# Kernel optimization log

Hardware: AMD Instinct MI355X
Metric: run time of the kernel (lower is better)

Reference implementation:

```python
import jax, jax.numpy as jnp
import numpy as np

N_NODES = 100_000
N_EDGES = 600_000
D = 128  # in_channels


def setup_inputs() -> dict:
    key = jax.random.key(0)
    k1, k2, k3, k4, k5 = jax.random.split(key, 5)
    node_embs_src = jax.random.normal(k1, (N_NODES, D), dtype=jnp.float32)
    node_embs_dst = jax.random.normal(k2, (N_NODES, D), dtype=jnp.float32)
    edge_index = jax.random.randint(k3, (2, N_EDGES), 0, N_NODES, dtype=jnp.int64)
    # MLP params: Linear(2D -> D), Linear(D -> 1); scaled like default torch init
    W1 = jax.random.normal(k4, (2 * D, D), dtype=jnp.float32) / np.sqrt(2 * D)
    b1 = jnp.zeros((D,), dtype=jnp.float32)
    W2 = jax.random.normal(k5, (D, 1), dtype=jnp.float32) / np.sqrt(D)
    b2 = jnp.zeros((1,), dtype=jnp.float32)
    return {
        "node_embs_src": node_embs_src,
        "node_embs_dst": node_embs_dst,
        "edge_index": edge_index,
        "W1": W1,
        "b1": b1,
        "W2": W2,
        "b2": b2,
    }


def reference(node_embs_src, node_embs_dst, edge_index, W1, b1, W2, b2):
    # Gather per-edge source / destination embeddings: [E, D] each
    src = node_embs_src[edge_index[0]]
    dst = node_embs_dst[edge_index[1]]
    # concat([src, dst]) @ W1 == src @ W1[:D] + dst @ W1[D:]  (avoids materializing [E, 2D])
    h = jnp.dot(src, W1[:D]) + jnp.dot(dst, W1[D:]) + b1  # [E, D]
    h = jax.nn.relu(h)
    logits = jnp.dot(h, W2) + b2  # [E, 1]
    return jax.nn.sigmoid(logits)
```

## Files before the change

kernel.cpp:

```cpp
#include <hip/hip_runtime.h>
#include <stdint.h>

typedef __attribute__((ext_vector_type(8))) short short8;
typedef __attribute__((ext_vector_type(4))) float f32x4;

__device__ __forceinline__ unsigned short f2bf(float f) {
  union { float f; uint32_t u; } v; v.f = f;
  uint32_t u = v.u;
  uint32_t r = (u + 0x7FFFu + ((u >> 16) & 1u)) >> 16;
  return (unsigned short)r;
}
__device__ __forceinline__ float bf2f(unsigned short h) {
  union { uint32_t u; float f; } v; v.u = ((uint32_t)h) << 16; return v.f;
}

#define NBM 64
__global__ __launch_bounds__(256, 4)
void node_phase_kernel(const float* __restrict__ src_emb,
                       const float* __restrict__ dst_emb,
                       const float* __restrict__ W1,
                       unsigned short* __restrict__ UV,
                       int Nn, int ntiles) {
  __shared__ __align__(16) char Als[NBM * 256];

  const int tbl = blockIdx.y;
  const float* emb = tbl ? dst_emb : src_emb;
  const float* Wt  = W1 + (size_t)tbl * 128 * 128;
  unsigned short* outp = UV + (size_t)tbl * Nn * 128;

  const int tid  = threadIdx.x;
  const int lane = tid & 63;
  const int w    = tid >> 6;
  const int l15  = lane & 15;
  const int lk8  = (lane >> 4) * 8;

  short8 bfrag[4][2];
#pragma unroll
  for (int s = 0; s < 4; ++s) {
#pragma unroll
    for (int nf = 0; nf < 2; ++nf) {
      const int col = w * 32 + 2 * l15 + nf;
      short8 t;
#pragma unroll
      for (int j = 0; j < 8; ++j) {
        const int k = s * 32 + lk8 + j;
        t[j] = (short)f2bf(Wt[k * 128 + col]);
      }
      bfrag[s][nf] = t;
    }
  }

  const int q = tid & 15, r0 = tid >> 4;
  const int swz = (l15 & 7) << 4;
  const int gx = gridDim.x;

  float4 p0[4], p1[4];
#pragma unroll
  for (int i = 0; i < 4; ++i) {
    const int node = blockIdx.x * NBM + i * 16 + r0;
    if (node < Nn) {
      const float* base = emb + (size_t)node * 128 + q * 8;
      p0[i] = *(const float4*)base;
      p1[i] = *(const float4*)(base + 4);
    }
  }

  for (int t = blockIdx.x; t < ntiles; t += gx) {
    const int t0 = t * NBM;

#pragma unroll
    for (int i = 0; i < 4; ++i) {
      const int row = i * 16 + r0;
      short8 hv;
      hv[0] = (short)f2bf(p0[i].x); hv[1] = (short)f2bf(p0[i].y);
      hv[2] = (short)f2bf(p0[i].z); hv[3] = (short)f2bf(p0[i].w);
      hv[4] = (short)f2bf(p1[i].x); hv[5] = (short)f2bf(p1[i].y);
      hv[6] = (short)f2bf(p1[i].z); hv[7] = (short)f2bf(p1[i].w);
      const int byteoff = row * 256 + ((q * 16) ^ ((row & 7) << 4));
      *(short8*)(Als + byteoff) = hv;
    }
    __syncthreads();

    const int tn = t + gx;
    if (tn < ntiles) {
#pragma unroll
      for (int i = 0; i < 4; ++i) {
        const int node = tn * NBM + i * 16 + r0;
        if (node < Nn) {
          const float* base = emb + (size_t)node * 128 + q * 8;
          p0[i] = *(const float4*)base;
          p1[i] = *(const float4*)(base + 4);
        }
      }
    }

#pragma unroll
    for (int m = 0; m < 4; ++m) {
      f32x4 acc0 = {0.f, 0.f, 0.f, 0.f};
      f32x4 acc1 = {0.f, 0.f, 0.f, 0.f};
      const int rowb = (m * 16 + l15) * 256;
      const int kb0  = lk8 * 2;
#pragma unroll
      for (int s = 0; s < 4; ++s) {
        const int off = rowb + ((s * 64 + kb0) ^ swz);
        const short8 a = *(const short8*)(Als + off);
        acc0 = __builtin_amdgcn_mfma_f32_16x16x32_bf16(a, bfrag[s][0], acc0, 0, 0, 0);
        acc1 = __builtin_amdgcn_mfma_f32_16x16x32_bf16(a, bfrag[s][1], acc1, 0, 0, 0);
      }
      const int col0 = w * 32 + 2 * l15;
#pragma unroll
      for (int reg = 0; reg < 4; ++reg) {
        const int orow = t0 + m * 16 + ((lane >> 4) * 4) + reg;
        if (orow < Nn) {
          const uint32_t pk = (uint32_t)f2bf(acc0[reg]) |
                              ((uint32_t)f2bf(acc1[reg]) << 16);
          *(uint32_t*)&outp[(size_t)orow * 128 + col0] = pk;
        }
      }
    }
    __syncthreads();
  }
}

__global__ __launch_bounds__(256, 8)
void edge_phase_kernel(const unsigned short* __restrict__ UV,
                       const int* __restrict__ eidx,
                       const float* __restrict__ b1,
                       const float* __restrict__ W2,
                       const float* __restrict__ b2,
                       float* __restrict__ out,
                       int E, int Nn) {
  const int tid = threadIdx.x;
  const int l15 = tid & 15;
  const int sg  = tid >> 4;

  float b1s[8], w2s[8];
#pragma unroll
  for (int j = 0; j < 8; ++j) {
    b1s[j] = b1[l15 * 8 + j];
    w2s[j] = W2[l15 * 8 + j];
  }
  const float b2s = b2[0];
  const unsigned short* U = UV;
  const unsigned short* V = UV + (size_t)Nn * 128;
  const int stride = gridDim.x * 16;

#pragma unroll 2
  for (int e = blockIdx.x * 16 + sg; e < E; e += stride) {
    const int s = eidx[e];
    const int d = eidx[E + e];
    const short8 u8 = *(const short8*)(U + (size_t)s * 128 + l15 * 8);
    const short8 v8 = *(const short8*)(V + (size_t)d * 128 + l15 * 8);
    float acc = 0.f;
#pragma unroll
    for (int j = 0; j < 8; ++j) {
      float g = bf2f((unsigned short)u8[j]) + bf2f((unsigned short)v8[j]) + b1s[j];
      g = g > 0.f ? g : 0.f;
      acc = fmaf(g, w2s[j], acc);
    }
#pragma unroll
    for (int off = 1; off < 16; off <<= 1)
      acc += __shfl_xor(acc, off, 64);
    if (l15 == 0) out[e] = 1.f / (1.f + __expf(-acc));
  }
}

#define BM 64
__global__ __launch_bounds__(256, 4)
void edge_decoder_fused(const float* __restrict__ src_emb,
                        const float* __restrict__ dst_emb,
                        const int* __restrict__ eidx,
                        const float* __restrict__ W1,
                        const float* __restrict__ b1,
                        const float* __restrict__ W2,
                        const float* __restrict__ b2,
                        float* __restrict__ out,
                        int E, int ntiles) {
  __shared__ __align__(16) char Als[BM * 512];
  __shared__ float rowpart[4][BM];

  const int tid  = threadIdx.x;
  const int lane = tid & 63;
  const int w    = tid >> 6;
  const int l15  = lane & 15;
  const int lk8  = (lane >> 4) * 8;

  short8 bfrag[8][2];
#pragma unroll
  for (int s = 0; s < 8; ++s) {
#pragma unroll
    for (int nf = 0; nf < 2; ++nf) {
      const int col = w * 32 + nf * 16 + l15;
      short8 t;
#pragma unroll
      for (int j = 0; j < 8; ++j) {
        const int k = s * 32 + lk8 + j;
        t[j] = (short)f2bf(W1[k * 128 + col]);
      }
      bfrag[s][nf] = t;
    }
  }
  float b1v[2], w2v[2];
#pragma unroll
  for (int nf = 0; nf < 2; ++nf) {
    const int col = w * 32 + nf * 16 + l15;
    b1v[nf] = b1[col];
    w2v[nf] = W2[col];
  }
  const float b2s = b2[0];

  const int q  = tid & 31;
  const int r0 = tid >> 5;
  const int qq = q & 15;
  const bool is_src = (q < 16);
  const int swz = (l15 & 7) << 4;

  for (int t = blockIdx.x; t < ntiles; t += gridDim.x) {
    const int t0 = t * BM;
#pragma unroll
    for (int i = 0; i < 8; ++i) {
      const int row = i * 8 + r0;
      const int e = t0 + row;
      if (e < E) {
        const int node = is_src ? eidx[e] : eidx[E + e];
        const float* base = (is_src ? src_emb : dst_emb) + (size_t)node * 128 + qq * 8;
        const float4 f0 = *(const float4*)base;
        const float4 f1 = *(const float4*)(base + 4);
        short8 hv;
        hv[0] = (short)f2bf(f0.x); hv[1] = (short)f2bf(f0.y);
        hv[2] = (short)f2bf(f0.z); hv[3] = (short)f2bf(f0.w);
        hv[4] = (short)f2bf(f1.x); hv[5] = (short)f2bf(f1.y);
        hv[6] = (short)f2bf(f1.z); hv[7] = (short)f2bf(f1.w);
        const int byteoff = row * 512 + ((q * 16) ^ ((row & 7) << 4));
        *(short8*)(Als + byteoff) = hv;
      }
    }
    __syncthreads();

    for (int m = 0; m < 4; ++m) {
      f32x4 acc0 = {0.f, 0.f, 0.f, 0.f};
      f32x4 acc1 = {0.f, 0.f, 0.f, 0.f};
      const int rowb = (m * 16 + l15) * 512;
      const int kb0  = lk8 * 2;
#pragma unroll
      for (int s = 0; s < 8; ++s) {
        const int off = rowb + ((s * 64 + kb0) ^ swz);
        const short8 a = *(const short8*)(Als + off);
        acc0 = __builtin_amdgcn_mfma_f32_16x16x32_bf16(a, bfrag[s][0], acc0, 0, 0, 0);
        acc1 = __builtin_amdgcn_mfma_f32_16x16x32_bf16(a, bfrag[s][1], acc1, 0, 0, 0);
      }
      float pr[4];
#pragma unroll
      for (int reg = 0; reg < 4; ++reg) {
        float h0 = acc0[reg] + b1v[0]; h0 = h0 > 0.f ? h0 : 0.f;
        float h1 = acc1[reg] + b1v[1]; h1 = h1 > 0.f ? h1 : 0.f;
        pr[reg] = h0 * w2v[0] + h1 * w2v[1];
      }
#pragma unroll
      for (int off = 1; off < 16; off <<= 1) {
#pragma unroll
        for (int reg = 0; reg < 4; ++reg)
          pr[reg] += __shfl_xor(pr[reg], off, 64);
      }
      if (l15 == 0) {
        const int rbase = m * 16 + (lane >> 4) * 4;
#pragma unroll
        for (int reg = 0; reg < 4; ++reg)
          rowpart[w][rbase + reg] = pr[reg];
      }
    }
    __syncthreads();

    if (tid < BM) {
      const int e = t0 + tid;
      if (e < E) {
        const float sum = rowpart[0][tid] + rowpart[1][tid] +
                          rowpart[2][tid] + rowpart[3][tid] + b2s;
        out[e] = 1.f / (1.f + __expf(-sum));
      }
    }
    __syncthreads();
  }
}

extern "C" void kernel_launch(void* const* d_in, const int* in_sizes, int n_in,
                              void* d_out, int out_size, void* d_ws, size_t ws_size,
                              hipStream_t stream) {
  const float* src = (const float*)d_in[0];
  const float* dst = (const float*)d_in[1];
  const int*   eix = (const int*)d_in[2];
  const float* W1  = (const float*)d_in[3];
  const float* b1  = (const float*)d_in[4];
  const float* W2  = (const float*)d_in[5];
  const float* b2  = (const float*)d_in[6];
  float* out = (float*)d_out;

  const int E  = in_sizes[2] / 2;
  const int Nn = in_sizes[0] / 128;
  const size_t uv_bytes = (size_t)Nn * 128 * 2 * sizeof(unsigned short);

  if (ws_size >= uv_bytes) {
    unsigned short* UV = (unsigned short*)d_ws;
    const int ntiles_n = (Nn + NBM - 1) / NBM;
    const int gx = ntiles_n < 512 ? ntiles_n : 512;
    node_phase_kernel<<<dim3(gx, 2), 256, 0, stream>>>(src, dst, W1, UV, Nn, ntiles_n);
    const int nblk = ((E + 15) / 16 < 2048) ? (E + 15) / 16 : 2048;
    edge_phase_kernel<<<nblk, 256, 0, stream>>>(UV, eix, b1, W2, b2, out, E, Nn);
  } else {
    const int ntiles = (E + BM - 1) / BM;
    const int grid = ntiles < 2048 ? ntiles : 2048;
    edge_decoder_fused<<<grid, 256, 0, stream>>>(src, dst, eix, W1, b1, W2, b2,
                                                 out, E, ntiles);
  }
}
```

Baseline: 76.02 us.

## Fold b1 into node phase and double-buffer edge gathers

```diff
diff --git a/kernel.cpp b/kernel.cpp
--- a/kernel.cpp
+++ b/kernel.cpp
@@ -19,6 +19,7 @@
 void node_phase_kernel(const float* __restrict__ src_emb,
                        const float* __restrict__ dst_emb,
                        const float* __restrict__ W1,
+                       const float* __restrict__ b1,
                        unsigned short* __restrict__ UV,
                        int Nn, int ntiles) {
   __shared__ __align__(16) char Als[NBM * 256];
@@ -49,6 +50,9 @@
       bfrag[s][nf] = t;
     }
   }
+  const int colb = w * 32 + 2 * l15;
+  const float bias0 = tbl ? 0.f : b1[colb];
+  const float bias1 = tbl ? 0.f : b1[colb + 1];
 
   const int q = tid & 15, r0 = tid >> 4;
   const int swz = (l15 & 7) << 4;
@@ -107,25 +111,58 @@
         acc0 = __builtin_amdgcn_mfma_f32_16x16x32_bf16(a, bfrag[s][0], acc0, 0, 0, 0);
         acc1 = __builtin_amdgcn_mfma_f32_16x16x32_bf16(a, bfrag[s][1], acc1, 0, 0, 0);
       }
-      const int col0 = w * 32 + 2 * l15;
 #pragma unroll
       for (int reg = 0; reg < 4; ++reg) {
         const int orow = t0 + m * 16 + ((lane >> 4) * 4) + reg;
         if (orow < Nn) {
-          const uint32_t pk = (uint32_t)f2bf(acc0[reg]) |
-                              ((uint32_t)f2bf(acc1[reg]) << 16);
-          *(uint32_t*)&outp[(size_t)orow * 128 + col0] = pk;
+          const uint32_t pk = (uint32_t)f2bf(acc0[reg] + bias0) |
+                              ((uint32_t)f2bf(acc1[reg] + bias1) << 16);
+          *(uint32_t*)&outp[(size_t)orow * 128 + colb] = pk;
         }
       }
     }
     __syncthreads();
   }
 }
+
+#define PREFETCH_PAIR(eL, su0, sv0, su1, sv1)                                  \
+  {                                                                            \
+    const int _e0 = (eL), _e1 = (eL) + stride;                                 \
+    const int _i0 = _e0 < E ? _e0 : 0;                                         \
+    const int _i1 = _e1 < E ? _e1 : 0;                                         \
+    const uint32_t _s0 = (uint32_t)eidx[_i0], _d0 = (uint32_t)eidx[E + _i0];   \
+    const uint32_t _s1 = (uint32_t)eidx[_i1], _d1 = (uint32_t)eidx[E + _i1];   \
+    su0 = *(const short8*)(U + (size_t)_s0 * 128 + l15 * 8);                   \
+    sv0 = *(const short8*)(V + (size_t)_d0 * 128 + l15 * 8);                   \
+    su1 = *(const short8*)(U + (size_t)_s1 * 128 + l15 * 8);                   \
+    sv1 = *(const short8*)(V + (size_t)_d1 * 128 + l15 * 8);                   \
+  }
+
+#define COMPUTE_PAIR(eL, su0, sv0, su1, sv1)                                   \
+  {                                                                            \
+    float _a0 = 0.f, _a1 = 0.f;                                                \
+    _Pragma("unroll") for (int _c = 0; _c < 8; ++_c) {                         \
+      float _g0 = bf2f((unsigned short)su0[_c]) + bf2f((unsigned short)sv0[_c]); \
+      float _g1 = bf2f((unsigned short)su1[_c]) + bf2f((unsigned short)sv1[_c]); \
+      _g0 = _g0 > 0.f ? _g0 : 0.f;                                             \
+      _g1 = _g1 > 0.f ? _g1 : 0.f;                                             \
+      _a0 = fmaf(_g0, w2s[_c], _a0);                                           \
+      _a1 = fmaf(_g1, w2s[_c], _a1);                                           \
+    }                                                                          \
+    _Pragma("unroll") for (int _off = 1; _off < 16; _off <<= 1) {              \
+      _a0 += __shfl_xor(_a0, _off, 64);                                        \
+      _a1 += __shfl_xor(_a1, _off, 64);                                        \
+    }                                                                          \
+    if (l15 == 0) {                                                            \
+      const int _e0 = (eL), _e1 = (eL) + stride;                               \
+      if (_e0 < E) out[_e0] = 1.f / (1.f + __expf(-(_a0 + b2s)));              \
+      if (_e1 < E) out[_e1] = 1.f / (1.f + __expf(-(_a1 + b2s)));              \
+    }                                                                          \
+  }
 
 __global__ __launch_bounds__(256, 8)
 void edge_phase_kernel(const unsigned short* __restrict__ UV,
                        const int* __restrict__ eidx,
-                       const float* __restrict__ b1,
                        const float* __restrict__ W2,
                        const float* __restrict__ b2,
                        float* __restrict__ out,
@@ -134,34 +171,37 @@
   const int l15 = tid & 15;
   const int sg  = tid >> 4;
 
-  float b1s[8], w2s[8];
-#pragma unroll
-  for (int j = 0; j < 8; ++j) {
-    b1s[j] = b1[l15 * 8 + j];
-    w2s[j] = W2[l15 * 8 + j];
-  }
+  float w2s[8];
+#pragma unroll
+  for (int j = 0; j < 8; ++j) w2s[j] = W2[l15 * 8 + j];
   const float b2s = b2[0];
   const unsigned short* U = UV;
   const unsigned short* V = UV + (size_t)Nn * 128;
+
   const int stride = gridDim.x * 16;
-
-#pragma unroll 2
-  for (int e = blockIdx.x * 16 + sg; e < E; e += stride) {
-    const int s = eidx[e];
-    const int d = eidx[E + e];
-    const short8 u8 = *(const short8*)(U + (size_t)s * 128 + l15 * 8);
-    const short8 v8 = *(const short8*)(V + (size_t)d * 128 + l15 * 8);
-    float acc = 0.f;
-#pragma unroll
-    for (int j = 0; j < 8; ++j) {
-      float g = bf2f((unsigned short)u8[j]) + bf2f((unsigned short)v8[j]) + b1s[j];
-      g = g > 0.f ? g : 0.f;
-      acc = fmaf(g, w2s[j], acc);
-    }
-#pragma unroll
-    for (int off = 1; off < 16; off <<= 1)
-      acc += __shfl_xor(acc, off, 64);
-    if (l15 == 0) out[e] = 1.f / (1.f + __expf(-acc));
+  const int step   = stride * 2;
+
+  int e_lo = blockIdx.x * 16 + sg;
+
+  short8 uA0, vA0, uA1, vA1;
+  short8 uB0, vB0, uB1, vB1;
+  PREFETCH_PAIR(e_lo, uA0, vA0, uA1, vA1);
+
+  for (;;) {
+    {
+      const int e_nxt = e_lo + step;
+      PREFETCH_PAIR(e_nxt, uB0, vB0, uB1, vB1);
+      COMPUTE_PAIR(e_lo, uA0, vA0, uA1, vA1);
+      e_lo = e_nxt;
+      if (e_lo >= E) break;
+    }
+    {
+      const int e_nxt = e_lo + step;
+      PREFETCH_PAIR(e_nxt, uA0, vA0, uA1, vA1);
+      COMPUTE_PAIR(e_lo, uB0, vB0, uB1, vB1);
+      e_lo = e_nxt;
+      if (e_lo >= E) break;
+    }
   }
 }
 
@@ -303,9 +343,9 @@
     unsigned short* UV = (unsigned short*)d_ws;
     const int ntiles_n = (Nn + NBM - 1) / NBM;
     const int gx = ntiles_n < 512 ? ntiles_n : 512;
-    node_phase_kernel<<<dim3(gx, 2), 256, 0, stream>>>(src, dst, W1, UV, Nn, ntiles_n);
+    node_phase_kernel<<<dim3(gx, 2), 256, 0, stream>>>(src, dst, W1, b1, UV, Nn, ntiles_n);
     const int nblk = ((E + 15) / 16 < 2048) ? (E + 15) / 16 : 2048;
-    edge_phase_kernel<<<nblk, 256, 0, stream>>>(UV, eix, b1, W2, b2, out, E, Nn);
+    edge_phase_kernel<<<nblk, 256, 0, stream>>>(UV, eix, W2, b2, out, E, Nn);
   } else {
     const int ntiles = (E + BM - 1) / BM;
     const int grid = ntiles < 2048 ? ntiles : 2048;
```

New measurement: 76.99 us. Within noise of the previous version (+1.3%).

## Quantize per-node projections to int8 with per-row scales for edge gather

Applied to the files above, without the earlier changes.

```diff
diff --git a/kernel.cpp b/kernel.cpp
--- a/kernel.cpp
+++ b/kernel.cpp
@@ -2,6 +2,7 @@
 #include <stdint.h>
 
 typedef __attribute__((ext_vector_type(8))) short short8;
+typedef __attribute__((ext_vector_type(8))) signed char schar8;
 typedef __attribute__((ext_vector_type(4))) float f32x4;
 
 __device__ __forceinline__ unsigned short f2bf(float f) {
@@ -16,17 +17,21 @@
 
 #define NBM 64
 __global__ __launch_bounds__(256, 4)
-void node_phase_kernel(const float* __restrict__ src_emb,
-                       const float* __restrict__ dst_emb,
-                       const float* __restrict__ W1,
-                       unsigned short* __restrict__ UV,
-                       int Nn, int ntiles) {
+void node_phase_q8(const float* __restrict__ src_emb,
+                   const float* __restrict__ dst_emb,
+                   const float* __restrict__ W1,
+                   const float* __restrict__ b1,
+                   int8_t* __restrict__ Q,
+                   float* __restrict__ SC,
+                   int Nn, int ntiles) {
   __shared__ __align__(16) char Als[NBM * 256];
+  __shared__ __align__(16) float pam[NBM][4];
 
   const int tbl = blockIdx.y;
   const float* emb = tbl ? dst_emb : src_emb;
   const float* Wt  = W1 + (size_t)tbl * 128 * 128;
-  unsigned short* outp = UV + (size_t)tbl * Nn * 128;
+  int8_t* Qt  = Q  + (size_t)tbl * Nn * 128;
+  float*  SCt = SC + (size_t)tbl * Nn;
 
   const int tid  = threadIdx.x;
   const int lane = tid & 63;
@@ -49,6 +54,9 @@
       bfrag[s][nf] = t;
     }
   }
+  const int colb = w * 32 + 2 * l15;
+  const float bias0 = tbl ? 0.f : b1[colb];
+  const float bias1 = tbl ? 0.f : b1[colb + 1];
 
   const int q = tid & 15, r0 = tid >> 4;
   const int swz = (l15 & 7) << 4;
@@ -94,6 +102,7 @@
       }
     }
 
+    f32x4 h0[4], h1[4];
 #pragma unroll
     for (int m = 0; m < 4; ++m) {
       f32x4 acc0 = {0.f, 0.f, 0.f, 0.f};
@@ -107,14 +116,37 @@
         acc0 = __builtin_amdgcn_mfma_f32_16x16x32_bf16(a, bfrag[s][0], acc0, 0, 0, 0);
         acc1 = __builtin_amdgcn_mfma_f32_16x16x32_bf16(a, bfrag[s][1], acc1, 0, 0, 0);
       }
-      const int col0 = w * 32 + 2 * l15;
 #pragma unroll
       for (int reg = 0; reg < 4; ++reg) {
-        const int orow = t0 + m * 16 + ((lane >> 4) * 4) + reg;
-        if (orow < Nn) {
-          const uint32_t pk = (uint32_t)f2bf(acc0[reg]) |
-                              ((uint32_t)f2bf(acc1[reg]) << 16);
-          *(uint32_t*)&outp[(size_t)orow * 128 + col0] = pk;
+        h0[m][reg] = acc0[reg] + bias0;
+        h1[m][reg] = acc1[reg] + bias1;
+        float pm = fmaxf(fabsf(h0[m][reg]), fabsf(h1[m][reg]));
+        pm = fmaxf(pm, __shfl_xor(pm, 1, 16));
+        pm = fmaxf(pm, __shfl_xor(pm, 2, 16));
+        pm = fmaxf(pm, __shfl_xor(pm, 4, 16));
+        pm = fmaxf(pm, __shfl_xor(pm, 8, 16));
+        if (l15 == 0) pam[m * 16 + (lane >> 4) * 4 + reg][w] = pm;
+      }
+    }
+    __syncthreads();
+
+#pragma unroll
+    for (int m = 0; m < 4; ++m) {
+#pragma unroll
+      for (int reg = 0; reg < 4; ++reg) {
+        const int row  = m * 16 + (lane >> 4) * 4 + reg;
+        const int node = t0 + row;
+        const f32x4 pa = *(const f32x4*)pam[row];
+        float am = fmaxf(fmaxf(pa[0], pa[1]), fmaxf(pa[2], pa[3]));
+        am = fmaxf(am, 1e-20f);
+        const float rq = 127.0f / am;
+        if (node < Nn) {
+          const int q0 = (int)rintf(h0[m][reg] * rq);
+          const int q1 = (int)rintf(h1[m][reg] * rq);
+          *(unsigned short*)(Qt + (size_t)node * 128 + colb) =
+              (unsigned short)((q0 & 255) | ((q1 & 255) << 8));
+          if ((tid & 15) == 0 && tid < 64)
+            SCt[node] = am * (1.0f / 127.0f);
         }
       }
     }
@@ -123,45 +155,45 @@
 }
 
 __global__ __launch_bounds__(256, 8)
-void edge_phase_kernel(const unsigned short* __restrict__ UV,
-                       const int* __restrict__ eidx,
-                       const float* __restrict__ b1,
-                       const float* __restrict__ W2,
-                       const float* __restrict__ b2,
-                       float* __restrict__ out,
-                       int E, int Nn) {
+void edge_phase_q8(const int8_t* __restrict__ Qu,
+                   const int8_t* __restrict__ Qv,
+                   const float* __restrict__ scu,
+                   const float* __restrict__ scv,
+                   const int* __restrict__ eidx,
+                   const float* __restrict__ W2,
+                   const float* __restrict__ b2,
+                   float* __restrict__ out,
+                   int E) {
   const int tid = threadIdx.x;
   const int l15 = tid & 15;
   const int sg  = tid >> 4;
 
-  float b1s[8], w2s[8];
-#pragma unroll
-  for (int j = 0; j < 8; ++j) {
-    b1s[j] = b1[l15 * 8 + j];
-    w2s[j] = W2[l15 * 8 + j];
-  }
+  float w2s[8];
+#pragma unroll
+  for (int j = 0; j < 8; ++j) w2s[j] = W2[l15 * 8 + j];
   const float b2s = b2[0];
-  const unsigned short* U = UV;
-  const unsigned short* V = UV + (size_t)Nn * 128;
   const int stride = gridDim.x * 16;
 
 #pragma unroll 2
   for (int e = blockIdx.x * 16 + sg; e < E; e += stride) {
     const int s = eidx[e];
     const int d = eidx[E + e];
-    const short8 u8 = *(const short8*)(U + (size_t)s * 128 + l15 * 8);
-    const short8 v8 = *(const short8*)(V + (size_t)d * 128 + l15 * 8);
+    const schar8 qu = *(const schar8*)(Qu + (size_t)s * 128 + l15 * 8);
+    const schar8 qv = *(const schar8*)(Qv + (size_t)d * 128 + l15 * 8);
+    const float su = scu[s];
+    const float sv = scv[d];
     float acc = 0.f;
 #pragma unroll
     for (int j = 0; j < 8; ++j) {
-      float g = bf2f((unsigned short)u8[j]) + bf2f((unsigned short)v8[j]) + b1s[j];
+      float g = (float)(int)qu[j] * su + (float)(int)qv[j] * sv;
       g = g > 0.f ? g : 0.f;
       acc = fmaf(g, w2s[j], acc);
     }
-#pragma unroll
-    for (int off = 1; off < 16; off <<= 1)
-      acc += __shfl_xor(acc, off, 64);
-    if (l15 == 0) out[e] = 1.f / (1.f + __expf(-acc));
+    acc += __shfl_xor(acc, 1, 16);
+    acc += __shfl_xor(acc, 2, 16);
+    acc += __shfl_xor(acc, 4, 16);
+    acc += __shfl_xor(acc, 8, 16);
+    if (l15 == 0) out[e] = 1.f / (1.f + __expf(-(acc + b2s)));
   }
 }
 
@@ -297,15 +329,19 @@
 
   const int E  = in_sizes[2] / 2;
   const int Nn = in_sizes[0] / 128;
-  const size_t uv_bytes = (size_t)Nn * 128 * 2 * sizeof(unsigned short);
-
-  if (ws_size >= uv_bytes) {
-    unsigned short* UV = (unsigned short*)d_ws;
+  const size_t q_bytes  = (size_t)2 * Nn * 128;
+  const size_t sc_bytes = (size_t)2 * Nn * sizeof(float);
+
+  if (ws_size >= q_bytes + sc_bytes) {
+    int8_t* Q  = (int8_t*)d_ws;
+    float*  SC = (float*)((char*)d_ws + q_bytes);
     const int ntiles_n = (Nn + NBM - 1) / NBM;
     const int gx = ntiles_n < 512 ? ntiles_n : 512;
-    node_phase_kernel<<<dim3(gx, 2), 256, 0, stream>>>(src, dst, W1, UV, Nn, ntiles_n);
-    const int nblk = ((E + 15) / 16 < 2048) ? (E + 15) / 16 : 2048;
-    edge_phase_kernel<<<nblk, 256, 0, stream>>>(UV, eix, b1, W2, b2, out, E, Nn);
+    node_phase_q8<<<dim3(gx, 2), 256, 0, stream>>>(src, dst, W1, b1, Q, SC, Nn, ntiles_n);
+    const int nchunks = (E + 15) / 16;
+    const int nblk = nchunks < 2048 ? nchunks : 2048;
+    edge_phase_q8<<<nblk, 256, 0, stream>>>(Q, Q + (size_t)Nn * 128, SC, SC + Nn,
+                                            eix, W2, b2, out, E);
   } else {
     const int ntiles = (E + BM - 1) / BM;
     const int grid = ntiles < 2048 ? ntiles : 2048;
```

After: 74.15 us. -2.4%, faster.
